# Optimization experiments

Measured on AMD Instinct MI355X. Metric: run time of the kernel, lower is better.

## Reference

```python
import jax, jax.numpy as jnp
import numpy as np

# ---- straight-through binary quantizers (custom VJP matches torch autograd.Functions) ----
@jax.custom_vjp
def bq(x):
    return jnp.sign(x)
def _bq_fwd(x):
    return jnp.sign(x), x
def _bq_bwd(x, g):
    return (g * ((x > -1.0) & (x < 1.0)).astype(g.dtype),)
bq.defvjp(_bq_fwd, _bq_bwd)

@jax.custom_vjp
def bq_quad(x):
    return jnp.sign(x)
def _bqq_fwd(x):
    return jnp.sign(x), x
def _bqq_bwd(x, g):
    return (jnp.maximum(2.0 - jnp.abs(2.0 * x), 0.0) * g,)
bq_quad.defvjp(_bqq_fwd, _bqq_bwd)

def bilinear(x, W, s, b):
    # BiLinear: row-centered sign weights scaled by learned per-row factor, sign activations
    Wc = W - jnp.mean(W, axis=-1, keepdims=True)
    Wb = s * bq(Wc)                      # (out, in)
    return bq(x) @ Wb.T + b

def selective_scan(u, delta, A, Bs, Cs, D, delta_bias):
    # u, delta: (B,K,Dn,L); A: (K,Dn,N); Bs,Cs: (B,K,N,L); D, delta_bias: (K,Dn)
    Bn, K, Dn, L = u.shape
    N = A.shape[-1]
    delta = jax.nn.softplus(delta + delta_bias[None, :, :, None])
    def step(h, inp):
        ut, dt, Bt, Ct = inp             # (B,K,Dn),(B,K,Dn),(B,K,N),(B,K,N)
        dA = jnp.exp(dt[..., None] * A[None])
        h = dA * h + (dt * ut)[..., None] * Bt[:, :, None, :]
        y = jnp.einsum('bkdn,bkn->bkd', h, Ct)
        return h, y
    h0 = jnp.zeros((Bn, K, Dn, N), u.dtype)
    _, ys = jax.lax.scan(step, h0,
                         (u.transpose(3, 0, 1, 2), delta.transpose(3, 0, 1, 2),
                          Bs.transpose(3, 0, 1, 2), Cs.transpose(3, 0, 1, 2)))
    y = ys.transpose(1, 2, 3, 0)         # (B,K,Dn,L)
    return y + D[None, :, :, None] * u

def _forward(x, W_in, b_in, s_in, move0_b, conv_W, conv_b, rp_b0, prelu_a, rp_b1,
             Wl, bl, sl, Wd, bd, sd, dt_bias, A_logs, Ds, ln_w, ln_b, W_out, b_out, s_out):
    Bn, H, Wi, dm = x.shape
    Dn = conv_W.shape[0]
    K = 4
    N = A_logs.shape[1]
    R = Wd.shape[2]
    L = H * Wi
    xz = bilinear(x, W_in, s_in, b_in)                  # (B,H,W,2*Dn)
    xp, z = jnp.split(xz, 2, axis=-1)
    xc = xp.transpose(0, 3, 1, 2)                       # (B,Dn,H,W)
    # BConv2d: move0 bias -> sign (quad STE) -> binary conv -> RPReLU -> residual
    t = bq_quad(xc + move0_b[None, :, None, None])
    sc = jax.lax.stop_gradient(jnp.mean(jnp.abs(conv_W), axis=(1, 2, 3), keepdims=True))
    cw = jnp.clip(conv_W, -1.0, 1.0)
    Wb = jax.lax.stop_gradient(sc * jnp.sign(conv_W) - cw) + cw
    t = jax.lax.conv_general_dilated(t, Wb, (1, 1), [(1, 1), (1, 1)],
                                     dimension_numbers=('NCHW', 'OIHW', 'NCHW'))
    t = t + conv_b[None, :, None, None]
    t = t + rp_b0[None, :, None, None]
    t = jnp.where(t >= 0, t, prelu_a[None, :, None, None] * t)
    t = t + rp_b1[None, :, None, None] + xc
    xconv = jax.nn.silu(t)
    # 4-direction scan inputs
    x_flat = xconv.reshape(Bn, Dn, L)
    x_tr = xconv.transpose(0, 1, 3, 2).reshape(Bn, Dn, L)
    x_hwwh = jnp.stack([x_flat, x_tr], axis=1)
    xs = jnp.concatenate([x_hwwh, jnp.flip(x_hwwh, axis=-1)], axis=1)   # (B,K,Dn,L)
    # NOTE: torch does .view(B,L,-1) on contiguous (B,Dn,L) slices = raw reshape (not transpose)
    xin = xs.reshape(Bn, K, L, Dn)
    x_dbl = jax.vmap(bilinear, in_axes=(1, 0, 0, 0), out_axes=1)(xin, Wl, sl, bl)  # (B,K,L,R+2N)
    x_dbl = x_dbl.transpose(0, 1, 3, 2)                                 # (B,K,R+2N,L)
    dts_r, Bs, Cs = jnp.split(x_dbl, [R, R + N], axis=2)
    dts_in = dts_r.reshape(Bn, K, L, R)  # raw reshape, matches torch .view
    dts = jax.vmap(bilinear, in_axes=(1, 0, 0, 0), out_axes=1)(dts_in, Wd, sd, bd)  # (B,K,L,Dn)
    dts = dts.transpose(0, 1, 3, 2)                                     # (B,K,Dn,L)
    A = -jnp.exp(A_logs).reshape(K, Dn, N)
    out_y = selective_scan(xs, dts, A, Bs, Cs, Ds.reshape(K, Dn), dt_bias.reshape(K, Dn))
    inv_y = jnp.flip(out_y[:, 2:4], axis=-1)
    wh_y = out_y[:, 1].reshape(Bn, Dn, Wi, H).transpose(0, 1, 3, 2).reshape(Bn, Dn, L)
    invwh_y = inv_y[:, 1].reshape(Bn, Dn, Wi, H).transpose(0, 1, 3, 2).reshape(Bn, Dn, L)
    y = out_y[:, 0] + inv_y[:, 0] + wh_y + invwh_y                      # (B,Dn,L)
    y = y.transpose(0, 2, 1).reshape(Bn, H, Wi, Dn)
    mu = jnp.mean(y, axis=-1, keepdims=True)
    var = jnp.var(y, axis=-1, keepdims=True)
    y = (y - mu) / jnp.sqrt(var + 1e-5) * ln_w + ln_b                   # LayerNorm eps=1e-5
    y = y * jax.nn.silu(z)
    return bilinear(y, W_out, s_out, b_out)

def setup_inputs():
    key = jax.random.key(0)
    ks = jax.random.split(key, 12)
    B, H, Wi, dm = 4, 64, 64, 96
    Dn, N, R, K = 192, 16, 6, 4
    u = lambda k, sh, a: jax.random.uniform(k, sh, jnp.float32, -a, a)
    x = jax.random.normal(ks[0], (B, H, Wi, dm), jnp.float32)
    W_in = u(ks[1], (2 * Dn, dm), 0.015)
    b_in = u(ks[2], (2 * Dn,), 0.01)
    s_in = jnp.mean(jnp.abs(W_in), axis=1, keepdims=True)
    move0_b = jnp.zeros((Dn,), jnp.float32)
    conv_W = 0.05 * jax.random.normal(ks[3], (Dn, Dn, 3, 3), jnp.float32)
    conv_b = u(ks[4], (Dn,), 0.01)
    rp_b0 = jnp.zeros((Dn,), jnp.float32)
    prelu_a = 0.25 * jnp.ones((Dn,), jnp.float32)
    rp_b1 = jnp.zeros((Dn,), jnp.float32)
    Wl = u(ks[5], (K, R + 2 * N, Dn), 0.015)
    bl = u(ks[6], (K, R + 2 * N), 0.01)
    sl = jnp.mean(jnp.abs(Wl), axis=2, keepdims=True)
    std = R ** -0.5
    Wd = u(ks[7], (K, Dn, R), std)
    bd = u(ks[8], (K, Dn), 0.01)
    sd = jnp.mean(jnp.abs(Wd), axis=2, keepdims=True)
    dt = jnp.exp(jax.random.uniform(ks[9], (K * Dn,), jnp.float32)
                 * (np.log(0.1) - np.log(0.001)) + np.log(0.001))
    dt = jnp.clip(dt, 1e-4, None)
    dt_bias = dt + jnp.log(-jnp.expm1(-dt))
    A_logs = jnp.tile(jnp.log(jnp.arange(1, N + 1, dtype=jnp.float32))[None, :], (K * Dn, 1))
    Ds = jnp.ones((K * Dn,), jnp.float32)
    ln_w = jnp.ones((Dn,), jnp.float32)
    ln_b = jnp.zeros((Dn,), jnp.float32)
    W_out = u(ks[10], (dm, Dn), 0.015)
    b_out = u(ks[11], (dm,), 0.01)
    s_out = jnp.mean(jnp.abs(W_out), axis=1, keepdims=True)
    return dict(x=x, W_in=W_in, b_in=b_in, s_in=s_in, move0_b=move0_b, conv_W=conv_W,
                conv_b=conv_b, rp_b0=rp_b0, prelu_a=prelu_a, rp_b1=rp_b1, Wl=Wl, bl=bl,
                sl=sl, Wd=Wd, bd=bd, sd=sd, dt_bias=dt_bias, A_logs=A_logs, Ds=Ds,
                ln_w=ln_w, ln_b=ln_b, W_out=W_out, b_out=b_out, s_out=s_out)

def reference(x, W_in, b_in, s_in, move0_b, conv_W, conv_b, rp_b0, prelu_a, rp_b1,
              Wl, bl, sl, Wd, bd, sd, dt_bias, A_logs, Ds, ln_w, ln_b, W_out, b_out, s_out):
    return _forward(x, W_in, b_in, s_in, move0_b, conv_W, conv_b, rp_b0, prelu_a, rp_b1,
                    Wl, bl, sl, Wd, bd, sd, dt_bias, A_logs, Ds, ln_w, ln_b, W_out, b_out, s_out)
```

## Files before the change

### kernel.cpp

```cpp
#include <hip/hip_runtime.h>
#include <math.h>
#include <stdint.h>

#define BB 4
#define HH 64
#define WW2 64
#define DM 96
#define DN 192
#define KK 4
#define NN 16
#define RR 6
#define LL 4096
#define RN 38

#define LOG2E 1.4426950408889634f
#define LN2   0.6931471805599453f

#define OFF_WDB      0
#define OFF_WCS      4608
#define OFF_WAUX     15360
#define OFF_WSC      16896
#define OFF_WBIB     17088
#define OFF_WOUTB    18240
#define OFF_WLBB     18816
#define OFF_XBP      19728
#define OFF_PXS      19728
#define OFF_PXIN     412944
#define OFF_XP       462096
#define OFF_XCONV    3607824
#define OFF_XCT      6753552
#define OFF_HEND     462096
#define OFF_YA       9899280
#define OFF_SSUM     22482192

#define PLANE 4356
#define NCH 128
#define CHUNK 32

__device__ __forceinline__ float softplusf(float v) {
  return fmaxf(v, 0.f) + LN2 * log2f(1.f + exp2f(-fabsf(v) * LOG2E));
}
__device__ __forceinline__ float siluf(float v) {
  return v / (1.f + expf(-v));
}
__device__ __forceinline__ float waveAllSum(float s) {
  #pragma unroll
  for (int off = 32; off; off >>= 1) s += __shfl_xor(s, off, 64);
  return s;
}

__global__ __launch_bounds__(64) void k_prep(
    const float* __restrict__ W_in, const float* __restrict__ s_in,
    const float* __restrict__ W_out, const float* __restrict__ s_out,
    const float* __restrict__ Wl, const float* __restrict__ sl,
    const float* __restrict__ Wd, const float* __restrict__ sd,
    const float* __restrict__ convW, float* __restrict__ ws) {
  __shared__ float srow[1728];
  int r = blockIdx.x, lane = threadIdx.x;
  if (r < 384) {
    const float* row = W_in + r * DM;
    float s = 0.f;
    for (int c = lane; c < DM; c += 64) s += row[c];
    s = waveAllSum(s);
    float mean = s / (float)DM;
    if (lane < 3) {
      uint32_t wv = 0;
      #pragma unroll
      for (int i = 0; i < 32; ++i) wv |= (row[lane * 32 + i] - mean > 0.f ? 1u : 0u) << i;
      ((uint32_t*)(ws + OFF_WBIB))[r * 3 + lane] = wv;
    }
  } else if (r < 480) {
    int m = r - 384;
    const float* row = W_out + m * DN;
    float s = 0.f;
    for (int c = lane; c < DN; c += 64) s += row[c];
    s = waveAllSum(s);
    float mean = s / (float)DN;
    if (lane < 6) {
      uint32_t wv = 0;
      #pragma unroll
      for (int i = 0; i < 32; ++i) wv |= (row[lane * 32 + i] - mean > 0.f ? 1u : 0u) << i;
      ((uint32_t*)(ws + OFF_WOUTB))[m * 6 + lane] = wv;
    }
  } else if (r < 632) {
    int idx = r - 480;
    const float* row = Wl + idx * DN;
    float s = 0.f;
    for (int c = lane; c < DN; c += 64) s += row[c];
    s = waveAllSum(s);
    float mean = s / (float)DN;
    if (lane < 6) {
      uint32_t wv = 0;
      #pragma unroll
      for (int i = 0; i < 32; ++i) wv |= (row[lane * 32 + i] - mean > 0.f ? 1u : 0u) << i;
      ((uint32_t*)(ws + OFF_WLBB))[idx * 6 + lane] = wv;
    }
  } else if (r < 1400) {
    int idx = r - 632;
    const float* row = Wd + idx * RR;
    float s = (lane < RR) ? row[lane] : 0.f;
    s = waveAllSum(s);
    float mean = s / (float)RR;
    unsigned long long mb = __ballot((lane < RR) && (row[lane] - mean > 0.f));
    if (lane == 0) {
      ((uint32_t*)(ws + OFF_WDB))[idx] = (uint32_t)mb & 0x3Fu;
      (ws + OFF_WDB)[768 + idx] = sd[idx];
    }
  } else if (r < 1592) {
    int o = r - 1400;
    const float* row = convW + o * 1728;
    float s = 0.f;
    for (int j = lane; j < 1728; j += 64) {
      float v = row[j];
      srow[j] = v;
      s += fabsf(v);
    }
    s = waveAllSum(s);
    __syncthreads();
    float sc = s / 1728.f;
    uint32_t* wb = (uint32_t*)(ws + OFF_WCS);
    int* aux = (int*)(ws + OFF_WAUX);
    float* scf = ws + OFF_WSC;
    uint32_t word = 0;
    if (lane < 54) {
      int cw = lane / 9, tap = lane % 9;
      #pragma unroll
      for (int i = 0; i < 32; ++i)
        word |= (srow[(cw * 32 + i) * 9 + tap] > 0.f ? 1u : 0u) << i;
      wb[o * 56 + lane] = word;
    } else if (lane < 56) {
      wb[o * 56 + lane] = 0u;
    }
    int pc = (lane < 54) ? 2 * (int)__popc(word) - 32 : 0;
    int tapid = lane % 9;
    int wst = 0;
    #pragma unroll
    for (int cw = 0; cw < 6; ++cw) wst += __shfl(pc, cw * 9 + tapid, 64);
    int w_t[9];
    #pragma unroll
    for (int t9 = 0; t9 < 9; ++t9) w_t[t9] = __shfl(wst, t9, 64);
    if (lane == 0) {
      aux[o * 8 + 0] = w_t[0] + w_t[3] + w_t[6];
      aux[o * 8 + 1] = w_t[2] + w_t[5] + w_t[8];
      aux[o * 8 + 2] = w_t[0] + w_t[1] + w_t[2];
      aux[o * 8 + 3] = w_t[6] + w_t[7] + w_t[8];
      aux[o * 8 + 4] = w_t[0];
      aux[o * 8 + 5] = w_t[2];
      aux[o * 8 + 6] = w_t[6];
      aux[o * 8 + 7] = w_t[8];
      scf[o] = sc;
    }
  } else {
    int p = r - 1592;
    uint32_t* plane = (uint32_t*)(ws + OFF_XBP) + (size_t)p * PLANE;
    for (int i = lane; i < 66; i += 64) {
      plane[i] = 0u;
      plane[65 * 66 + i] = 0u;
    }
    for (int i = lane; i < 64; i += 64) {
      plane[(i + 1) * 66] = 0u;
      plane[(i + 1) * 66 + 65] = 0u;
    }
  }
}

__global__ __launch_bounds__(384) void k_bilin_in(
    const float* __restrict__ x, const float* __restrict__ b_in,
    const float* __restrict__ s_in, const float* __restrict__ move0,
    const float* __restrict__ ws, float* __restrict__ xp,
    uint32_t* __restrict__ pxin, uint32_t* __restrict__ xb) {
  __shared__ uint32_t spx[16 * 3];
  __shared__ float sxz[192 * 17];
  __shared__ float smv[DN];
  int p0 = blockIdx.x * 16;
  if (threadIdx.x < 48) {
    int pix = threadIdx.x / 3, wd = threadIdx.x % 3;
    const float* base = x + (size_t)(p0 + pix) * DM + wd * 32;
    uint32_t wv = 0;
    #pragma unroll
    for (int i = 0; i < 32; ++i) wv |= (base[i] > 0.f ? 1u : 0u) << i;
    spx[pix * 3 + wd] = wv;
  }
  if (threadIdx.x < DN) smv[threadIdx.x] = move0[threadIdx.x];
  __syncthreads();
  int half = threadIdx.x / 192;
  int o = threadIdx.x - half * 192;
  uint32_t w0, w1, w2;
  {
    const uint32_t* wb = (const uint32_t*)(ws + OFF_WBIB) + o * 3;
    w0 = wb[0]; w1 = wb[1]; w2 = wb[2];
  }
  float bias = b_in[o], sc = s_in[o];
  #pragma unroll
  for (int pp = 0; pp < 8; ++pp) {
    int pix = half * 8 + pp;
    int P = (int)__popc(spx[pix * 3 + 0] ^ w0) + (int)__popc(spx[pix * 3 + 1] ^ w1) +
            (int)__popc(spx[pix * 3 + 2] ^ w2);
    sxz[o * 17 + pix] = bias + sc * (float)(DM - 2 * P);
  }
  __syncthreads();
  int b = p0 >> 12, l0 = p0 & 4095;
  for (int f = threadIdx.x; f < DN * 16; f += 384) {
    int od = f >> 4, pix = f & 15;
    xp[((size_t)(b * DN + od)) * LL + l0 + pix] = sxz[od * 17 + pix];
  }
  if (threadIdx.x < 48) {
    int pix = threadIdx.x / 3, wd = threadIdx.x % 3;
    pxin[(size_t)(p0 + pix) * 3 + wd] = spx[pix * 3 + wd];
  }
  if (threadIdx.x < 96) {
    int pix = threadIdx.x / 6, cw = threadIdx.x % 6;
    uint32_t wv = 0;
    #pragma unroll
    for (int i = 0; i < 32; ++i) {
      int dch = cw * 32 + i;
      wv |= ((sxz[dch * 17 + pix] + smv[dch] > 0.f) ? 1u : 0u) << i;
    }
    int l = l0 + pix, h = l >> 6, w = l & 63;
    uint32_t* plane = xb + (size_t)(b * 6 + cw) * PLANE;
    plane[(h + 1) * 66 + 1 + w] = wv;
  }
}

__global__ __launch_bounds__(256) void k_conv(
    const uint32_t* __restrict__ xb, const float* __restrict__ xc,
    const uint32_t* __restrict__ wbits, const int* __restrict__ aux,
    const float* __restrict__ scf, const float* __restrict__ conv_b,
    const float* __restrict__ rp_b0, const float* __restrict__ prelu_a,
    const float* __restrict__ rp_b1, float* __restrict__ xconv) {
  int ocg = blockIdx.x & 3;
  int og = (blockIdx.x >> 2) & 3;
  int stripe = (blockIdx.x >> 4) & 15;
  int b = blockIdx.x >> 8;
  int w = threadIdx.x & 63, r = threadIdx.x >> 6;
  int h = stripe * 4 + r;
  int obase = og * 48 + ocg * 12;

  __shared__ uint32_t swb[12 * 56];
  __shared__ int saux[12 * 8];
  __shared__ float sconst[12 * 4];
  for (int i = threadIdx.x; i < 12 * 56; i += 256) swb[i] = wbits[obase * 56 + i];
  for (int i = threadIdx.x; i < 12 * 8; i += 256) saux[i] = aux[obase * 8 + i];
  if (threadIdx.x < 12) {
    int o = obase + threadIdx.x;
    sconst[threadIdx.x * 4 + 0] = scf[o];
    sconst[threadIdx.x * 4 + 1] = conv_b[o] + rp_b0[o];
    sconst[threadIdx.x * 4 + 2] = prelu_a[o];
    sconst[threadIdx.x * 4 + 3] = rp_b1[o];
  }

  uint32_t xw[6][9];
  const uint32_t* xpb = xb + (size_t)b * 6 * PLANE;
  #pragma unroll
  for (int cw = 0; cw < 6; ++cw) {
    const uint32_t* plane = xpb + cw * PLANE + (h + 1) * 66 + (w + 1);
    #pragma unroll
    for (int dy = 0; dy < 3; ++dy) {
      #pragma unroll
      for (int dx = 0; dx < 3; ++dx)
        xw[cw][dy * 3 + dx] = plane[(dy - 1) * 66 + (dx - 1)];
    }
  }
  bool isL = (w == 0), isR = (w == 63);
  bool isT = (h == 0), isB = (h == 63);
  const float* xcp = xc + ((size_t)(b * DN + obase)) * LL + h * 64 + w;
  float* xop = xconv + ((size_t)(b * DN + obase)) * LL + h * 64 + w;
  __syncthreads();

  #pragma unroll 1
  for (int oc = 0; oc < 12; ++oc) {
    const uint32_t* wp = &swb[oc * 56];
    int P = 0;
    #pragma unroll
    for (int cw = 0; cw < 6; ++cw) {
      int pp = 0;
      #pragma unroll
      for (int t = 0; t < 9; ++t) pp += (int)__popc(wp[cw * 9 + t] ^ xw[cw][t]);
      P += pp;
    }
    int corr = isL ? saux[oc * 8 + 0] : (isR ? saux[oc * 8 + 1] : 0);
    if (isT) {
      corr += saux[oc * 8 + 2];
      if (isL) corr -= saux[oc * 8 + 4];
      if (isR) corr -= saux[oc * 8 + 5];
    }
    if (isB) {
      corr += saux[oc * 8 + 3];
      if (isL) corr -= saux[oc * 8 + 6];
      if (isR) corr -= saux[oc * 8 + 7];
    }
    float acc = sconst[oc * 4 + 0] * (float)(1728 - 2 * P + corr);
    float t = acc + sconst[oc * 4 + 1];
    t = (t >= 0.f) ? t : sconst[oc * 4 + 2] * t;
    t += sconst[oc * 4 + 3] + *xcp;
    *xop = siluf(t);
    xcp += LL; xop += LL;
  }
}

__global__ __launch_bounds__(256) void k_bits_xpose(const float* __restrict__ xconv,
                                                    uint32_t* __restrict__ pxs,
                                                    float* __restrict__ xct) {
  __shared__ float tile[64][65];
  if (blockIdx.x < 768) {
    int bd = blockIdx.x;
    int b = bd / DN, dch = bd - b * DN;
    const float* img = xconv + (size_t)bd * LL;
    for (int i = threadIdx.x; i < LL; i += 256)
      tile[i >> 6][i & 63] = img[i];
    __syncthreads();
    int lane = threadIdx.x & 63;
    #pragma unroll
    for (int k = 0; k < 4; ++k) {
      size_t wbase = ((size_t)((b * KK + k) * DN + dch)) * 128;
      for (int j = threadIdx.x; j < LL; j += 256) {
        float v;
        if (k == 0)      v = tile[j >> 6][j & 63];
        else if (k == 1) v = tile[j & 63][j >> 6];
        else if (k == 2) { int t2 = 4095 - j; v = tile[t2 >> 6][t2 & 63]; }
        else             { int t2 = 4095 - j; v = tile[t2 & 63][t2 >> 6]; }
        unsigned long long m = __ballot(v > 0.f);
        if (lane == 0)       pxs[wbase + (j >> 5)] = (uint32_t)m;
        else if (lane == 32) pxs[wbase + (j >> 5)] = (uint32_t)(m >> 32);
      }
    }
  } else {
    int idx = blockIdx.x - 768;
    int ts = idx & 63;
    int rest = idx >> 6;
    int dg = rest % 3;
    int b = rest / 3;
    int d0 = dg * 64, t0 = ts * 64;
    for (int i = threadIdx.x; i < 4096; i += 256) {
      int dd = i >> 6, tt = i & 63;
      tile[dd][tt] = xconv[((size_t)(b * DN + d0 + dd)) * LL + t0 + tt];
    }
    __syncthreads();
    for (int i = threadIdx.x; i < 4096; i += 256) {
      int tt = i >> 6, dd = i & 63;
      xct[((size_t)(b * LL + t0 + tt)) * DN + d0 + dd] = tile[dd][tt];
    }
  }
}

__device__ __forceinline__ void rpowers(float r, float* a) {
  float r2 = r * r, r3 = r2 * r, r4 = r2 * r2, r8 = r4 * r4;
  a[0] = r;       a[1] = r2;      a[2] = r3;      a[3] = r4;
  a[4] = r4 * r;  a[5] = r4 * r2; a[6] = r4 * r3; a[7] = r8;
  a[8] = r8 * r;  a[9] = r8 * r2; a[10] = r8 * r3; a[11] = r8 * r4;
  a[12] = r8 * a[4]; a[13] = r8 * a[5]; a[14] = r8 * a[6]; a[15] = r8 * r8;
}

__device__ __forceinline__ int rowstep(int k) {
  return (k == 0) ? DN : (k == 1) ? 64 * DN : (k == 2) ? -DN : -64 * DN;
}

__global__ __launch_bounds__(192) void k_scan_a(
    const float* __restrict__ xct, const uint32_t* __restrict__ pxs,
    const float* __restrict__ ws, const float* __restrict__ bl,
    const float* __restrict__ sl, const float* __restrict__ bd,
    const float* __restrict__ dt_bias, const float* __restrict__ A_logs,
    const float* __restrict__ Ds, float* __restrict__ yA,
    float* __restrict__ hend, float* __restrict__ Ssum) {
  int c = blockIdx.x & (NCH - 1);
  int bk = blockIdx.x >> 7;
  int k = bk & 3, b = bk >> 2;
  int d = threadIdx.x;
  int t0 = c << 5;
  __shared__ uint32_t sdtm[CHUNK];
  __shared__ uint32_t spxr[CHUNK * 6];
  __shared__ uint32_t swl[RN * 6];
  __shared__ float sblv[RN], sslv[RN];
  __shared__ float4 sB4[CHUNK * 4];
  __shared__ float4 sC4[CHUNK * 4];
  float* sBf = (float*)sB4;
  float* sCf = (float*)sC4;
  const uint32_t* ppx = pxs + (size_t)bk * 24576;
  spxr[d] = ppx[t0 * 6 + d];
  for (int i = d; i < RN * 6; i += 192) swl[i] = ((const uint32_t*)(ws + OFF_WLBB))[k * RN * 6 + i];
  if (d < RN) {
    sblv[d] = bl[k * RN + d];
    sslv[d] = sl[k * RN + d];
  }
  __syncthreads();
  if (d < CHUNK) {
    uint32_t m = 0;
    int fbase = (t0 + d) * 6;
    #pragma unroll
    for (int r = 0; r < 6; ++r) {
      int f = fbase + r;
      int o = f >> 12, l = f & 4095;
      const uint32_t* prow = ppx + l * 6;
      int P = 0;
      #pragma unroll
      for (int j = 0; j < 6; ++j) P += (int)__popc(prow[j] ^ swl[o * 6 + j]);
      float val = sblv[o] + sslv[o] * (float)(DN - 2 * P);
      m |= (val > 0.f ? 1u : 0u) << r;
    }
    sdtm[d] = m;
  }
  for (int i = d; i < CHUNK * 32; i += 192) {
    int t = i >> 5, nn = i & 31;
    int o = RR + nn;
    int P = 0;
    #pragma unroll
    for (int j = 0; j < 6; ++j) P += (int)__popc(spxr[t * 6 + j] ^ swl[o * 6 + j]);
    float val = sblv[o] + sslv[o] * (float)(DN - 2 * P);
    if (nn < 16) sBf[t * 16 + nn] = val;
    else         sCf[t * 16 + (nn - 16)] = val;
  }
  uint32_t w6 = ((const uint32_t*)(ws + OFF_WDB))[k * DN + d];
  float sdvv = (ws + OFF_WDB)[768 + k * DN + d];
  float biasd = bd[k * DN + d] + dt_bias[k * DN + d];
  float Dd = Ds[k * DN + d];
  float Araw[16];
  bool fok = true;
  {
    const float* ap = A_logs + (k * DN + d) * NN;
    #pragma unroll
    for (int n = 0; n < NN; ++n) {
      Araw[n] = -expf(ap[n]);
      fok = fok && (fabsf(Araw[n] + (float)(n + 1)) < 1e-3f);
    }
  }
  bool fastpath = (__ballot(fok) == ~0ull);
  float An[16];
  if (!fastpath) {
    #pragma unroll
    for (int n = 0; n < NN; ++n) An[n] = Araw[n] * LOG2E;
  }
  float h[16];
  #pragma unroll
  for (int n = 0; n < NN; ++n) h[n] = 0.f;
  float S = 0.f;
  int ubase = b * (LL * DN) + d;
  int ybase = bk * (LL * DN) + d;
  int rstep = rowstep(k);
  __syncthreads();
  #pragma unroll 1
  for (int seg = 0; seg < 4; ++seg) {
    int tb = t0 + seg * 8;
    int r0 = (k >= 2) ? (4095 - tb) : tb;
    if (k & 1) r0 = ((r0 & 63) << 6) | (r0 >> 6);
    int rbase = r0 * DN;
    float uu[8];
    #pragma unroll
    for (int i = 0; i < 8; ++i) uu[i] = xct[ubase + rbase + i * rstep];
    #pragma unroll
    for (int i = 0; i < 8; ++i) {
      int t = seg * 8 + i;
      float uv = uu[i];
      int pc = (int)__popc(sdtm[t] ^ w6);
      float dv = softplusf(biasd + sdvv * (float)(RR - 2 * pc));
      S += dv;
      float du = dv * uv;
      float yv = Dd * uv;
      if (fastpath) {
        float rv = exp2f(-dv * LOG2E);
        float a[16];
        rpowers(rv, a);
        #pragma unroll
        for (int g = 0; g < 4; ++g) {
          float4 bv = sB4[t * 4 + g];
          float4 cv = sC4[t * 4 + g];
          h[4 * g + 0] = a[4 * g + 0] * h[4 * g + 0] + du * bv.x;
          h[4 * g + 1] = a[4 * g + 1] * h[4 * g + 1] + du * bv.y;
          h[4 * g + 2] = a[4 * g + 2] * h[4 * g + 2] + du * bv.z;
          h[4 * g + 3] = a[4 * g + 3] * h[4 * g + 3] + du * bv.w;
          yv += cv.x * h[4 * g + 0];
          yv += cv.y * h[4 * g + 1];
          yv += cv.z * h[4 * g + 2];
          yv += cv.w * h[4 * g + 3];
        }
      } else {
        #pragma unroll
        for (int g = 0; g < 4; ++g) {
          float4 bv = sB4[t * 4 + g];
          float4 cv = sC4[t * 4 + g];
          float a0 = exp2f(dv * An[4 * g + 0]);
          float a1 = exp2f(dv * An[4 * g + 1]);
          float a2 = exp2f(dv * An[4 * g + 2]);
          float a3 = exp2f(dv * An[4 * g + 3]);
          h[4 * g + 0] = a0 * h[4 * g + 0] + du * bv.x;
          h[4 * g + 1] = a1 * h[4 * g + 1] + du * bv.y;
          h[4 * g + 2] = a2 * h[4 * g + 2] + du * bv.z;
          h[4 * g + 3] = a3 * h[4 * g + 3] + du * bv.w;
          yv += cv.x * h[4 * g + 0];
          yv += cv.y * h[4 * g + 1];
          yv += cv.z * h[4 * g + 2];
          yv += cv.w * h[4 * g + 3];
        }
      }
      yA[ybase + rbase + i * rstep] = yv;
    }
  }
  float* hp = hend + (size_t)c * 49152 + (size_t)(bk * DN + d) * 16;
  #pragma unroll
  for (int n = 0; n < NN; n += 4)
    *(float4*)(hp + n) = make_float4(h[n], h[n + 1], h[n + 2], h[n + 3]);
  Ssum[c * 3072 + bk * DN + d] = S;
}

__global__ __launch_bounds__(256) void k_scan_b(
    const float* __restrict__ A_logs, const float* __restrict__ Ssum,
    float* __restrict__ hend) {
  int tid = blockIdx.x * 256 + threadIdx.x;
  int bkd = tid >> 4, n = tid & 15;
  int bk = bkd / DN, d = bkd - bk * DN;
  int k = bk & 3;
  float An2 = -expf(A_logs[(k * DN + d) * NN + n]) * LOG2E;
  float h = 0.f;
  float Sc = Ssum[bkd];
  float he = hend[tid];
  #pragma unroll 1
  for (int c = 0; c < NCH; ++c) {
    float Sn = 0.f, hn = 0.f;
    if (c < NCH - 1) {
      Sn = Ssum[(c + 1) * 3072 + bkd];
      hn = hend[(size_t)(c + 1) * 49152 + tid];
    }
    hend[(size_t)c * 49152 + tid] = h;
    h = exp2f(An2 * Sc) * h + he;
    Sc = Sn; he = hn;
  }
}

__global__ __launch_bounds__(192) void k_scan_corr(
    float* __restrict__ yA, const uint32_t* __restrict__ pxs,
    const float* __restrict__ ws, const float* __restrict__ bl,
    const float* __restrict__ sl, const float* __restrict__ bd,
    const float* __restrict__ dt_bias, const float* __restrict__ A_logs,
    const float* __restrict__ h0buf) {
  int c = blockIdx.x & (NCH - 1);
  if (c == 0) return;
  int bk = blockIdx.x >> 7;
  int k = bk & 3;
  int d = threadIdx.x;
  int t0 = c << 5;
  __shared__ uint32_t sdtm[CHUNK];
  __shared__ uint32_t spxr[CHUNK * 6];
  __shared__ uint32_t swl[RN * 6];
  __shared__ float sblv[RN], sslv[RN];
  __shared__ float4 sC4[CHUNK * 4];
  float* sCf = (float*)sC4;
  const uint32_t* ppx = pxs + (size_t)bk * 24576;
  spxr[d] = ppx[t0 * 6 + d];
  for (int i = d; i < RN * 6; i += 192) swl[i] = ((const uint32_t*)(ws + OFF_WLBB))[k * RN * 6 + i];
  if (d < RN) {
    sblv[d] = bl[k * RN + d];
    sslv[d] = sl[k * RN + d];
  }
  __syncthreads();
  if (d < CHUNK) {
    uint32_t m = 0;
    int fbase = (t0 + d) * 6;
    #pragma unroll
    for (int r = 0; r < 6; ++r) {
      int f = fbase + r;
      int o = f >> 12, l = f & 4095;
      const uint32_t* prow = ppx + l * 6;
      int P = 0;
      #pragma unroll
      for (int j = 0; j < 6; ++j) P += (int)__popc(prow[j] ^ swl[o * 6 + j]);
      float val = sblv[o] + sslv[o] * (float)(DN - 2 * P);
      m |= (val > 0.f ? 1u : 0u) << r;
    }
    sdtm[d] = m;
  }
  for (int i = d; i < CHUNK * 16; i += 192) {
    int t = i >> 4, n = i & 15;
    int o = RR + NN + n;
    int P = 0;
    #pragma unroll
    for (int j = 0; j < 6; ++j) P += (int)__popc(spxr[t * 6 + j] ^ swl[o * 6 + j]);
    sCf[t * 16 + n] = sblv[o] + sslv[o] * (float)(DN - 2 * P);
  }
  uint32_t w6 = ((const uint32_t*)(ws + OFF_WDB))[k * DN + d];
  float sdvv = (ws + OFF_WDB)[768 + k * DN + d];
  float biasd = bd[k * DN + d] + dt_bias[k * DN + d];
  float Araw[16];
  bool fok = true;
  {
    const float* ap = A_logs + (k * DN + d) * NN;
    #pragma unroll
    for (int n = 0; n < NN; ++n) {
      Araw[n] = -expf(ap[n]);
      fok = fok && (fabsf(Araw[n] + (float)(n + 1)) < 1e-3f);
    }
  }
  bool fastpath = (__ballot(fok) == ~0ull);
  float An[16];
  if (!fastpath) {
    #pragma unroll
    for (int n = 0; n < NN; ++n) An[n] = Araw[n] * LOG2E;
  }
  float h0[16];
  {
    const float* hp = h0buf + (size_t)c * 49152 + (size_t)(bk * DN + d) * 16;
    #pragma unroll
    for (int n = 0; n < NN; n += 4) {
      float4 v = *(const float4*)(hp + n);
      h0[n] = v.x; h0[n + 1] = v.y; h0[n + 2] = v.z; h0[n + 3] = v.w;
    }
  }
  float S = 0.f;
  int ybase = bk * (LL * DN) + d;
  int rstep = rowstep(k);
  __syncthreads();
  #pragma unroll 1
  for (int seg = 0; seg < 4; ++seg) {
    int tb = t0 + seg * 8;
    int r0 = (k >= 2) ? (4095 - tb) : tb;
    if (k & 1) r0 = ((r0 & 63) << 6) | (r0 >> 6);
    int rbase = r0 * DN;
    float yy[8];
    #pragma unroll
    for (int i = 0; i < 8; ++i) yy[i] = yA[ybase + rbase + i * rstep];
    #pragma unroll
    for (int i = 0; i < 8; ++i) {
      int t = seg * 8 + i;
      int pc = (int)__popc(sdtm[t] ^ w6);
      S += softplusf(biasd + sdvv * (float)(RR - 2 * pc));
      float yv = 0.f;
      if (fastpath) {
        float rho = exp2f(-S * LOG2E);
        float a[16];
        rpowers(rho, a);
        #pragma unroll
        for (int g = 0; g < 4; ++g) {
          float4 cv = sC4[t * 4 + g];
          yv += cv.x * (a[4 * g + 0] * h0[4 * g + 0]);
          yv += cv.y * (a[4 * g + 1] * h0[4 * g + 1]);
          yv += cv.z * (a[4 * g + 2] * h0[4 * g + 2]);
          yv += cv.w * (a[4 * g + 3] * h0[4 * g + 3]);
        }
      } else {
        #pragma unroll
        for (int g = 0; g < 4; ++g) {
          float4 cv = sC4[t * 4 + g];
          yv += cv.x * (exp2f(S * An[4 * g + 0]) * h0[4 * g + 0]);
          yv += cv.y * (exp2f(S * An[4 * g + 1]) * h0[4 * g + 1]);
          yv += cv.z * (exp2f(S * An[4 * g + 2]) * h0[4 * g + 2]);
          yv += cv.w * (exp2f(S * An[4 * g + 3]) * h0[4 * g + 3]);
        }
      }
      yA[ybase + rbase + i * rstep] = yy[i] + yv;
    }
  }
}

__global__ __launch_bounds__(256) void k_ln_out(
    const float* __restrict__ yA, const uint32_t* __restrict__ pxin,
    const float* __restrict__ b_in, const float* __restrict__ s_in,
    const float* __restrict__ ln_w, const float* __restrict__ ln_b,
    const float* __restrict__ ws, const float* __restrict__ b_out,
    const float* __restrict__ s_out, float* __restrict__ out) {
  __shared__ float ty[16 * 193];
  __shared__ float ps[256];
  __shared__ float smu[16], srs[16];
  __shared__ float slw[DN], slb[DN];
  __shared__ uint32_t ybits[16 * 6];
  __shared__ uint32_t swo[96 * 6];
  __shared__ float sb[96], ssc[96];
  __shared__ uint32_t szw[DN * 3];
  __shared__ float szb[DN], szs[DN];
  __shared__ uint32_t spxt[16 * 3];
  int b = blockIdx.x >> 8;
  int l0 = (blockIdx.x & 255) << 4;
  if (threadIdx.x < DN) {
    slw[threadIdx.x] = ln_w[threadIdx.x];
    slb[threadIdx.x] = ln_b[threadIdx.x];
    szb[threadIdx.x] = b_in[DN + threadIdx.x];
    szs[threadIdx.x] = s_in[DN + threadIdx.x];
  }
  for (int i = threadIdx.x; i < 96 * 6; i += 256) swo[i] = ((const uint32_t*)(ws + OFF_WOUTB))[i];
  for (int i = threadIdx.x; i < DN * 3; i += 256) szw[i] = ((const uint32_t*)(ws + OFF_WBIB))[DN * 3 + i];
  if (threadIdx.x < 96) {
    sb[threadIdx.x] = b_out[threadIdx.x];
    ssc[threadIdx.x] = s_out[threadIdx.x];
  }
  if (threadIdx.x < 48) spxt[threadIdx.x] = pxin[(size_t)(b * LL + l0) * 3 + threadIdx.x];
  const float* y0 = yA + (size_t)(b * 4 + 0) * (LL * DN) + (size_t)l0 * DN;
  const float* y1 = yA + (size_t)(b * 4 + 1) * (LL * DN) + (size_t)l0 * DN;
  const float* y2 = yA + (size_t)(b * 4 + 2) * (LL * DN) + (size_t)l0 * DN;
  const float* y3 = yA + (size_t)(b * 4 + 3) * (LL * DN) + (size_t)l0 * DN;
  for (int i = threadIdx.x; i < 16 * DN; i += 256) {
    int lc = i / DN, dd = i - lc * DN;
    size_t off = (size_t)lc * DN + dd;
    ty[lc * 193 + dd] = y0[off] + y1[off] + y2[off] + y3[off];
  }
  __syncthreads();
  int lc = threadIdx.x & 15, part = threadIdx.x >> 4;
  float s = 0.f;
  for (int d = part * 12; d < part * 12 + 12; ++d) s += ty[lc * 193 + d];
  ps[threadIdx.x] = s;
  __syncthreads();
  if (threadIdx.x < 16) {
    float m = 0.f;
    #pragma unroll
    for (int p = 0; p < 16; ++p) m += ps[p * 16 + threadIdx.x];
    smu[threadIdx.x] = m / (float)DN;
  }
  __syncthreads();
  float mu = smu[lc];
  float q = 0.f;
  for (int d = part * 12; d < part * 12 + 12; ++d) {
    float v = ty[lc * 193 + d] - mu; q += v * v;
  }
  ps[threadIdx.x] = q;
  __syncthreads();
  if (threadIdx.x < 16) {
    float vv = 0.f;
    #pragma unroll
    for (int p = 0; p < 16; ++p) vv += ps[p * 16 + threadIdx.x];
    srs[threadIdx.x] = rsqrtf(vv / (float)DN + 1e-5f);
  }
  __syncthreads();
  if (threadIdx.x < 16 * 6) {
    int lc2 = threadIdx.x / 6, wd = threadIdx.x % 6;
    float mu2 = smu[lc2], rs2 = srs[lc2];
    uint32_t px0 = spxt[lc2 * 3 + 0], px1 = spxt[lc2 * 3 + 1], px2 = spxt[lc2 * 3 + 2];
    uint32_t wv = 0;
    #pragma unroll
    for (int i = 0; i < 32; ++i) {
      int dd = wd * 32 + i;
      float lnv = (ty[lc2 * 193 + dd] - mu2) * rs2 * slw[dd] + slb[dd];
      int P = (int)__popc(px0 ^ szw[dd * 3 + 0]) + (int)__popc(px1 ^ szw[dd * 3 + 1]) +
              (int)__popc(px2 ^ szw[dd * 3 + 2]);
      float zv = szb[dd] + szs[dd] * (float)(DM - 2 * P);
      wv |= ((lnv * zv > 0.f) ? 1u : 0u) << i;
    }
    ybits[lc2 * 6 + wd] = wv;
  }
  __syncthreads();
  float* op = out + (size_t)(b * LL + l0) * DM;
  for (int oi = threadIdx.x; oi < 16 * DM; oi += 256) {
    int pr = oi / DM, m = oi % DM;
    int P = 0;
    #pragma unroll
    for (int j = 0; j < 6; ++j) P += (int)__popc(ybits[pr * 6 + j] ^ swo[m * 6 + j]);
    op[(size_t)pr * DM + m] = sb[m] + ssc[m] * (float)(DN - 2 * P);
  }
}

extern "C" void kernel_launch(void* const* d_in, const int* in_sizes, int n_in,
                              void* d_out, int out_size, void* d_ws, size_t ws_size,
                              hipStream_t stream) {
  const float* x       = (const float*)d_in[0];
  const float* W_in    = (const float*)d_in[1];
  const float* b_in    = (const float*)d_in[2];
  const float* s_in    = (const float*)d_in[3];
  const float* move0_b = (const float*)d_in[4];
  const float* conv_W  = (const float*)d_in[5];
  const float* conv_b  = (const float*)d_in[6];
  const float* rp_b0   = (const float*)d_in[7];
  const float* prelu_a = (const float*)d_in[8];
  const float* rp_b1   = (const float*)d_in[9];
  const float* Wl      = (const float*)d_in[10];
  const float* bl      = (const float*)d_in[11];
  const float* sl      = (const float*)d_in[12];
  const float* Wd      = (const float*)d_in[13];
  const float* bd      = (const float*)d_in[14];
  const float* sd      = (const float*)d_in[15];
  const float* dt_bias = (const float*)d_in[16];
  const float* A_logs  = (const float*)d_in[17];
  const float* Ds      = (const float*)d_in[18];
  const float* ln_w    = (const float*)d_in[19];
  const float* ln_b    = (const float*)d_in[20];
  const float* W_out   = (const float*)d_in[21];
  const float* b_out   = (const float*)d_in[22];
  const float* s_out   = (const float*)d_in[23];
  float* ws  = (float*)d_ws;
  float* out = (float*)d_out;

  hipLaunchKernelGGL(k_prep, dim3(1616), dim3(64), 0, stream,
                     W_in, s_in, W_out, s_out, Wl, sl, Wd, sd, conv_W, ws);
  hipLaunchKernelGGL(k_bilin_in, dim3(1024), dim3(384), 0, stream,
                     x, b_in, s_in, move0_b, ws, ws + OFF_XP,
                     (uint32_t*)(ws + OFF_PXIN), (uint32_t*)(ws + OFF_XBP));
  hipLaunchKernelGGL(k_conv, dim3(1024), dim3(256), 0, stream,
                     (const uint32_t*)(ws + OFF_XBP), ws + OFF_XP,
                     (const uint32_t*)(ws + OFF_WCS), (const int*)(ws + OFF_WAUX),
                     ws + OFF_WSC, conv_b, rp_b0, prelu_a, rp_b1,
                     ws + OFF_XCONV);
  hipLaunchKernelGGL(k_bits_xpose, dim3(1536), dim3(256), 0, stream,
                     ws + OFF_XCONV, (uint32_t*)(ws + OFF_PXS), ws + OFF_XCT);
  hipLaunchKernelGGL(k_scan_a, dim3(2048), dim3(192), 0, stream,
                     ws + OFF_XCT, (const uint32_t*)(ws + OFF_PXS), ws, bl, sl,
                     bd, dt_bias, A_logs, Ds, ws + OFF_YA, ws + OFF_HEND,
                     ws + OFF_SSUM);
  hipLaunchKernelGGL(k_scan_b, dim3(192), dim3(256), 0, stream,
                     A_logs, ws + OFF_SSUM, ws + OFF_HEND);
  hipLaunchKernelGGL(k_scan_corr, dim3(2048), dim3(192), 0, stream,
                     ws + OFF_YA, (const uint32_t*)(ws + OFF_PXS), ws, bl, sl,
                     bd, dt_bias, A_logs, ws + OFF_HEND);
  hipLaunchKernelGGL(k_ln_out, dim3(1024), dim3(256), 0, stream,
                     ws + OFF_YA, (const uint32_t*)(ws + OFF_PXIN), b_in, s_in,
                     ln_w, ln_b, ws, b_out, s_out, out);
}
```

Measured before the change: 313.6 us.

## Restructure chunked scan: state-only first pass, full recompute pass from carried state

The first scan pass now computes only per-chunk end states and delta sums, dropping C projections and y output writes. The correction pass becomes a full rescan that starts from the carried-in chunk state, producing y directly with the D skip term, instead of reading back and patching a partial y. Softplus and exp of delta are precomputed into shared-memory lookup tables indexed by the 7 possible popcount values. This removes one full read/write of yA and the correction exponentials, at the cost of redoing the recurrence in the second pass.

```diff
diff --git a/kernel.cpp b/kernel.cpp
--- a/kernel.cpp
+++ b/kernel.cpp
@@ -354,13 +354,17 @@
 __device__ __forceinline__ int rowstep(int k) {
   return (k == 0) ? DN : (k == 1) ? 64 * DN : (k == 2) ? -DN : -64 * DN;
 }
+__device__ __forceinline__ int rowbase(int k, int tb) {
+  int r0 = (k >= 2) ? (4095 - tb) : tb;
+  if (k & 1) r0 = ((r0 & 63) << 6) | (r0 >> 6);
+  return r0 * DN;
+}
 
 __global__ __launch_bounds__(192) void k_scan_a(
     const float* __restrict__ xct, const uint32_t* __restrict__ pxs,
     const float* __restrict__ ws, const float* __restrict__ bl,
     const float* __restrict__ sl, const float* __restrict__ bd,
     const float* __restrict__ dt_bias, const float* __restrict__ A_logs,
-    const float* __restrict__ Ds, float* __restrict__ yA,
     float* __restrict__ hend, float* __restrict__ Ssum) {
   int c = blockIdx.x & (NCH - 1);
   int bk = blockIdx.x >> 7;
@@ -372,9 +376,8 @@
   __shared__ uint32_t swl[RN * 6];
   __shared__ float sblv[RN], sslv[RN];
   __shared__ float4 sB4[CHUNK * 4];
-  __shared__ float4 sC4[CHUNK * 4];
+  __shared__ float sDV[7 * 192], sR[7 * 192];
   float* sBf = (float*)sB4;
-  float* sCf = (float*)sC4;
   const uint32_t* ppx = pxs + (size_t)bk * 24576;
   spxr[d] = ppx[t0 * 6 + d];
   for (int i = d; i < RN * 6; i += 192) swl[i] = ((const uint32_t*)(ws + OFF_WLBB))[k * RN * 6 + i];
@@ -399,20 +402,23 @@
     }
     sdtm[d] = m;
   }
-  for (int i = d; i < CHUNK * 32; i += 192) {
-    int t = i >> 5, nn = i & 31;
-    int o = RR + nn;
+  for (int i = d; i < CHUNK * 16; i += 192) {
+    int t = i >> 4, n = i & 15;
+    int o = RR + n;
     int P = 0;
     #pragma unroll
     for (int j = 0; j < 6; ++j) P += (int)__popc(spxr[t * 6 + j] ^ swl[o * 6 + j]);
-    float val = sblv[o] + sslv[o] * (float)(DN - 2 * P);
-    if (nn < 16) sBf[t * 16 + nn] = val;
-    else         sCf[t * 16 + (nn - 16)] = val;
+    sBf[t * 16 + n] = sblv[o] + sslv[o] * (float)(DN - 2 * P);
   }
   uint32_t w6 = ((const uint32_t*)(ws + OFF_WDB))[k * DN + d];
   float sdvv = (ws + OFF_WDB)[768 + k * DN + d];
   float biasd = bd[k * DN + d] + dt_bias[k * DN + d];
-  float Dd = Ds[k * DN + d];
+  #pragma unroll
+  for (int pc = 0; pc < 7; ++pc) {
+    float dv = softplusf(biasd + sdvv * (float)(RR - 2 * pc));
+    sDV[pc * 192 + d] = dv;
+    sR[pc * 192 + d] = exp2f(-dv * LOG2E);
+  }
   float Araw[16];
   bool fok = true;
   {
@@ -434,15 +440,11 @@
   for (int n = 0; n < NN; ++n) h[n] = 0.f;
   float S = 0.f;
   int ubase = b * (LL * DN) + d;
-  int ybase = bk * (LL * DN) + d;
   int rstep = rowstep(k);
   __syncthreads();
   #pragma unroll 1
   for (int seg = 0; seg < 4; ++seg) {
-    int tb = t0 + seg * 8;
-    int r0 = (k >= 2) ? (4095 - tb) : tb;
-    if (k & 1) r0 = ((r0 & 63) << 6) | (r0 >> 6);
-    int rbase = r0 * DN;
+    int rbase = rowbase(k, t0 + seg * 8);
     float uu[8];
     #pragma unroll
     for (int i = 0; i < 8; ++i) uu[i] = xct[ubase + rbase + i * rstep];
@@ -451,32 +453,25 @@
       int t = seg * 8 + i;
       float uv = uu[i];
       int pc = (int)__popc(sdtm[t] ^ w6);
-      float dv = softplusf(biasd + sdvv * (float)(RR - 2 * pc));
+      float dv = sDV[pc * 192 + d];
       S += dv;
       float du = dv * uv;
-      float yv = Dd * uv;
       if (fastpath) {
-        float rv = exp2f(-dv * LOG2E);
+        float rv = sR[pc * 192 + d];
         float a[16];
         rpowers(rv, a);
         #pragma unroll
         for (int g = 0; g < 4; ++g) {
           float4 bv = sB4[t * 4 + g];
-          float4 cv = sC4[t * 4 + g];
           h[4 * g + 0] = a[4 * g + 0] * h[4 * g + 0] + du * bv.x;
           h[4 * g + 1] = a[4 * g + 1] * h[4 * g + 1] + du * bv.y;
           h[4 * g + 2] = a[4 * g + 2] * h[4 * g + 2] + du * bv.z;
           h[4 * g + 3] = a[4 * g + 3] * h[4 * g + 3] + du * bv.w;
-          yv += cv.x * h[4 * g + 0];
-          yv += cv.y * h[4 * g + 1];
-          yv += cv.z * h[4 * g + 2];
-          yv += cv.w * h[4 * g + 3];
         }
       } else {
         #pragma unroll
         for (int g = 0; g < 4; ++g) {
           float4 bv = sB4[t * 4 + g];
-          float4 cv = sC4[t * 4 + g];
           float a0 = exp2f(dv * An[4 * g + 0]);
           float a1 = exp2f(dv * An[4 * g + 1]);
           float a2 = exp2f(dv * An[4 * g + 2]);
@@ -485,13 +480,8 @@
           h[4 * g + 1] = a1 * h[4 * g + 1] + du * bv.y;
           h[4 * g + 2] = a2 * h[4 * g + 2] + du * bv.z;
           h[4 * g + 3] = a3 * h[4 * g + 3] + du * bv.w;
-          yv += cv.x * h[4 * g + 0];
-          yv += cv.y * h[4 * g + 1];
-          yv += cv.z * h[4 * g + 2];
-          yv += cv.w * h[4 * g + 3];
         }
       }
-      yA[ybase + rbase + i * rstep] = yv;
     }
   }
   float* hp = hend + (size_t)c * 49152 + (size_t)(bk * DN + d) * 16;
@@ -525,23 +515,26 @@
   }
 }
 
-__global__ __launch_bounds__(192) void k_scan_corr(
-    float* __restrict__ yA, const uint32_t* __restrict__ pxs,
+__global__ __launch_bounds__(192) void k_scan_c(
+    const float* __restrict__ xct, const uint32_t* __restrict__ pxs,
     const float* __restrict__ ws, const float* __restrict__ bl,
     const float* __restrict__ sl, const float* __restrict__ bd,
     const float* __restrict__ dt_bias, const float* __restrict__ A_logs,
+    const float* __restrict__ Ds, float* __restrict__ yA,
     const float* __restrict__ h0buf) {
   int c = blockIdx.x & (NCH - 1);
-  if (c == 0) return;
   int bk = blockIdx.x >> 7;
-  int k = bk & 3;
+  int k = bk & 3, b = bk >> 2;
   int d = threadIdx.x;
   int t0 = c << 5;
   __shared__ uint32_t sdtm[CHUNK];
   __shared__ uint32_t spxr[CHUNK * 6];
   __shared__ uint32_t swl[RN * 6];
   __shared__ float sblv[RN], sslv[RN];
+  __shared__ float4 sB4[CHUNK * 4];
   __shared__ float4 sC4[CHUNK * 4];
+  __shared__ float sDV[7 * 192], sR[7 * 192];
+  float* sBf = (float*)sB4;
   float* sCf = (float*)sC4;
   const uint32_t* ppx = pxs + (size_t)bk * 24576;
   spxr[d] = ppx[t0 * 6 + d];
@@ -567,17 +560,26 @@
     }
     sdtm[d] = m;
   }
-  for (int i = d; i < CHUNK * 16; i += 192) {
-    int t = i >> 4, n = i & 15;
-    int o = RR + NN + n;
+  for (int i = d; i < CHUNK * 32; i += 192) {
+    int t = i >> 5, nn = i & 31;
+    int o = RR + nn;
     int P = 0;
     #pragma unroll
     for (int j = 0; j < 6; ++j) P += (int)__popc(spxr[t * 6 + j] ^ swl[o * 6 + j]);
-    sCf[t * 16 + n] = sblv[o] + sslv[o] * (float)(DN - 2 * P);
+    float val = sblv[o] + sslv[o] * (float)(DN - 2 * P);
+    if (nn < 16) sBf[t * 16 + nn] = val;
+    else         sCf[t * 16 + (nn - 16)] = val;
   }
   uint32_t w6 = ((const uint32_t*)(ws + OFF_WDB))[k * DN + d];
   float sdvv = (ws + OFF_WDB)[768 + k * DN + d];
   float biasd = bd[k * DN + d] + dt_bias[k * DN + d];
+  float Dd = Ds[k * DN + d];
+  #pragma unroll
+  for (int pc = 0; pc < 7; ++pc) {
+    float dv = softplusf(biasd + sdvv * (float)(RR - 2 * pc));
+    sDV[pc * 192 + d] = dv;
+    sR[pc * 192 + d] = exp2f(-dv * LOG2E);
+  }
   float Araw[16];
   bool fok = true;
   {
@@ -594,57 +596,73 @@
     #pragma unroll
     for (int n = 0; n < NN; ++n) An[n] = Araw[n] * LOG2E;
   }
-  float h0[16];
+  float h[16];
   {
     const float* hp = h0buf + (size_t)c * 49152 + (size_t)(bk * DN + d) * 16;
     #pragma unroll
     for (int n = 0; n < NN; n += 4) {
       float4 v = *(const float4*)(hp + n);
-      h0[n] = v.x; h0[n + 1] = v.y; h0[n + 2] = v.z; h0[n + 3] = v.w;
-    }
-  }
-  float S = 0.f;
+      h[n] = v.x; h[n + 1] = v.y; h[n + 2] = v.z; h[n + 3] = v.w;
+    }
+  }
+  int ubase = b * (LL * DN) + d;
   int ybase = bk * (LL * DN) + d;
   int rstep = rowstep(k);
   __syncthreads();
   #pragma unroll 1
   for (int seg = 0; seg < 4; ++seg) {
-    int tb = t0 + seg * 8;
-    int r0 = (k >= 2) ? (4095 - tb) : tb;
-    if (k & 1) r0 = ((r0 & 63) << 6) | (r0 >> 6);
-    int rbase = r0 * DN;
-    float yy[8];
-    #pragma unroll
-    for (int i = 0; i < 8; ++i) yy[i] = yA[ybase + rbase + i * rstep];
+    int rbase = rowbase(k, t0 + seg * 8);
+    float uu[8];
+    #pragma unroll
+    for (int i = 0; i < 8; ++i) uu[i] = xct[ubase + rbase + i * rstep];
     #pragma unroll
     for (int i = 0; i < 8; ++i) {
       int t = seg * 8 + i;
+      float uv = uu[i];
       int pc = (int)__popc(sdtm[t] ^ w6);
-      S += softplusf(biasd + sdvv * (float)(RR - 2 * pc));
-      float yv = 0.f;
+      float dv = sDV[pc * 192 + d];
+      float du = dv * uv;
+      float p[4];
+      #pragma unroll
+      for (int g = 0; g < 4; ++g) p[g] = 0.f;
       if (fastpath) {
-        float rho = exp2f(-S * LOG2E);
+        float rv = sR[pc * 192 + d];
         float a[16];
-        rpowers(rho, a);
+        rpowers(rv, a);
         #pragma unroll
         for (int g = 0; g < 4; ++g) {
+          float4 bv = sB4[t * 4 + g];
           float4 cv = sC4[t * 4 + g];
-          yv += cv.x * (a[4 * g + 0] * h0[4 * g + 0]);
-          yv += cv.y * (a[4 * g + 1] * h0[4 * g + 1]);
-          yv += cv.z * (a[4 * g + 2] * h0[4 * g + 2]);
-          yv += cv.w * (a[4 * g + 3] * h0[4 * g + 3]);
+          h[4 * g + 0] = a[4 * g + 0] * h[4 * g + 0] + du * bv.x;
+          h[4 * g + 1] = a[4 * g + 1] * h[4 * g + 1] + du * bv.y;
+          h[4 * g + 2] = a[4 * g + 2] * h[4 * g + 2] + du * bv.z;
+          h[4 * g + 3] = a[4 * g + 3] * h[4 * g + 3] + du * bv.w;
+          p[g] += cv.x * h[4 * g + 0];
+          p[g] += cv.y * h[4 * g + 1];
+          p[g] += cv.z * h[4 * g + 2];
+          p[g] += cv.w * h[4 * g + 3];
         }
       } else {
         #pragma unroll
         for (int g = 0; g < 4; ++g) {
+          float4 bv = sB4[t * 4 + g];
           float4 cv = sC4[t * 4 + g];
-          yv += cv.x * (exp2f(S * An[4 * g + 0]) * h0[4 * g + 0]);
-          yv += cv.y * (exp2f(S * An[4 * g + 1]) * h0[4 * g + 1]);
-          yv += cv.z * (exp2f(S * An[4 * g + 2]) * h0[4 * g + 2]);
-          yv += cv.w * (exp2f(S * An[4 * g + 3]) * h0[4 * g + 3]);
+          float a0 = exp2f(dv * An[4 * g + 0]);
+          float a1 = exp2f(dv * An[4 * g + 1]);
+          float a2 = exp2f(dv * An[4 * g + 2]);
+          float a3 = exp2f(dv * An[4 * g + 3]);
+          h[4 * g + 0] = a0 * h[4 * g + 0] + du * bv.x;
+          h[4 * g + 1] = a1 * h[4 * g + 1] + du * bv.y;
+          h[4 * g + 2] = a2 * h[4 * g + 2] + du * bv.z;
+          h[4 * g + 3] = a3 * h[4 * g + 3] + du * bv.w;
+          p[g] += cv.x * h[4 * g + 0];
+          p[g] += cv.y * h[4 * g + 1];
+          p[g] += cv.z * h[4 * g + 2];
+          p[g] += cv.w * h[4 * g + 3];
         }
       }
-      yA[ybase + rbase + i * rstep] = yy[i] + yv;
+      float yv = Dd * uv + ((p[0] + p[1]) + (p[2] + p[3]));
+      yA[ybase + rbase + i * rstep] = yv;
     }
   }
 }
@@ -787,13 +805,12 @@
                      ws + OFF_XCONV, (uint32_t*)(ws + OFF_PXS), ws + OFF_XCT);
   hipLaunchKernelGGL(k_scan_a, dim3(2048), dim3(192), 0, stream,
                      ws + OFF_XCT, (const uint32_t*)(ws + OFF_PXS), ws, bl, sl,
-                     bd, dt_bias, A_logs, Ds, ws + OFF_YA, ws + OFF_HEND,
-                     ws + OFF_SSUM);
+                     bd, dt_bias, A_logs, ws + OFF_HEND, ws + OFF_SSUM);
   hipLaunchKernelGGL(k_scan_b, dim3(192), dim3(256), 0, stream,
                      A_logs, ws + OFF_SSUM, ws + OFF_HEND);
-  hipLaunchKernelGGL(k_scan_corr, dim3(2048), dim3(192), 0, stream,
-                     ws + OFF_YA, (const uint32_t*)(ws + OFF_PXS), ws, bl, sl,
-                     bd, dt_bias, A_logs, ws + OFF_HEND);
+  hipLaunchKernelGGL(k_scan_c, dim3(2048), dim3(192), 0, stream,
+                     ws + OFF_XCT, (const uint32_t*)(ws + OFF_PXS), ws, bl, sl,
+                     bd, dt_bias, A_logs, Ds, ws + OFF_YA, ws + OFF_HEND);
   hipLaunchKernelGGL(k_ln_out, dim3(1024), dim3(256), 0, stream,
                      ws + OFF_YA, (const uint32_t*)(ws + OFF_PXIN), b_in, s_in,
                      ln_w, ln_b, ws, b_out, s_out, out);
```

New measurement: 300.3 us. 1.04x faster.
